# Performance work log

Hardware: AMD Instinct MI355X
Metric: run time of the kernel (lower is better)

## Reference

```python
import jax, jax.numpy as jnp
import numpy as np

# Static config matching init_kwargs
NUM_EXPERTS = 8
CAP_FACTOR = 1.0
MIN_CAP = 8


def setup_inputs() -> dict:
    key = jax.random.key(0)
    ks = jax.random.split(key, 10)
    G, S, D, H, E = 4, 4096, 1024, 4096, NUM_EXPERTS
    s = 0.02  # init stddev like nn.initializers.normal(0.02)
    return {
        "x": jax.random.normal(ks[0], (G, S, D), dtype=jnp.float32),
        "gate": jax.random.normal(ks[1], (D, E), dtype=jnp.float32) * s,
        "W1": jax.random.normal(ks[2], (E, D, H), dtype=jnp.float32) * s,
        "b1": jnp.zeros((E, H), dtype=jnp.float32),
        "W2": jax.random.normal(ks[3], (E, H, D), dtype=jnp.float32) * s,
        "b2": jnp.zeros((E, D), dtype=jnp.float32),
        "Ws1": jax.random.normal(ks[4], (D, H), dtype=jnp.float32) * s,
        "bs1": jnp.zeros((H,), dtype=jnp.float32),
        "Ws2": jax.random.normal(ks[5], (H, D), dtype=jnp.float32) * s,
        "bs2": jnp.zeros((D,), dtype=jnp.float32),
    }


def reference(x, gate, W1, b1, W2, b2, Ws1, bs1, Ws2, bs2):
    G, S, D = x.shape
    E = gate.shape[1]
    T = G * S
    capacity = max(MIN_CAP, int(CAP_FACTOR * T / E))  # static -> 2048

    # ---- Router (inference path: indices + scores, loss = 0) ----
    logits = jnp.einsum('gsd,de->gse', x, gate)           # (G,S,E)
    probs = jax.nn.softmax(logits, axis=-1)
    flat_probs = probs.transpose(2, 0, 1).reshape(E, T)    # (E,T)
    # capacity <= T here, so padding width is 0 (kept implicit)
    scores, token_idx = jax.lax.top_k(flat_probs, k=capacity)  # (E,C)
    scores = jnp.where(scores > -1e8, scores, 0.0)

    # ---- Routed experts: gather -> per-expert FFN (grouped GEMM) -> scatter-add
    flat_x = x.reshape(T, D)
    tok = flat_x[token_idx]                                # (E,C,D) gather
    h = jax.nn.gelu(jnp.einsum('ecd,edh->ech', tok, W1) + b1[:, None, :])
    out_tok = jnp.einsum('ech,ehd->ecd', h, W2) + b2[:, None, :]
    scaled = out_tok * scores[..., None]                   # weight by routing prob
    routed = jnp.zeros_like(flat_x).at[token_idx.reshape(-1)].add(
        scaled.reshape(E * capacity, D)).reshape(G, S, D)

    # ---- Shared expert (single FFN applied to all tokens) ----
    shared = jax.nn.gelu(jnp.einsum('gsd,dh->gsh', x, Ws1) + bs1)
    shared = jnp.einsum('gsh,hd->gsd', shared, Ws2) + bs2

    return routed + shared
```

## Files before the change

kernel.cpp:

```cpp
#include <hip/hip_runtime.h>
#include <hip/hip_bf16.h>

using bf16 = __hip_bfloat16;
typedef short v8s __attribute__((ext_vector_type(8)));
typedef float v4f __attribute__((ext_vector_type(4)));

#define NE 8
#define NT 16384
#define ND 1024
#define NH 4096
#define CAP 2048

__device__ __forceinline__ void load_lds16(const void* g, void* s) {
  __builtin_amdgcn_global_load_lds(
      (const __attribute__((address_space(1))) unsigned int*)g,
      (__attribute__((address_space(3))) unsigned int*)s, 16, 0, 0);
}

__device__ __forceinline__ float gelu_tanh(float x) {
  float u = 0.7978845608028654f * (x + 0.044715f * x * x * x);
  float e = __expf(2.0f * u);
  float t = 1.0f - 2.0f / (e + 1.0f);
  return 0.5f * x * (1.0f + t);
}

__global__ __launch_bounds__(256) void cvt_bf16(const float* __restrict__ s,
                                                bf16* __restrict__ d, int n) {
  for (int i = (blockIdx.x * 256 + threadIdx.x) * 4; i < n; i += gridDim.x * 1024) {
    float4 v = *(const float4*)(s + i);
    bf16 o[4];
    o[0] = __float2bfloat16(v.x); o[1] = __float2bfloat16(v.y);
    o[2] = __float2bfloat16(v.z); o[3] = __float2bfloat16(v.w);
    *(ushort4*)(d + i) = *(ushort4*)o;
  }
}

__global__ __launch_bounds__(256) void tcvt(const float* __restrict__ src,
                                            bf16* __restrict__ dst, int R, int C) {
  __shared__ float tile[32][33];
  size_t mo = (size_t)blockIdx.z * R * C;
  int c0 = blockIdx.x * 32, r0 = blockIdx.y * 32;
  int tx = threadIdx.x & 31, ty = threadIdx.x >> 5;
  for (int i = ty; i < 32; i += 8)
    tile[i][tx] = src[mo + (size_t)(r0 + i) * C + c0 + tx];
  __syncthreads();
  for (int i = ty; i < 32; i += 8)
    dst[mo + (size_t)(c0 + i) * R + r0 + tx] = __float2bfloat16(tile[tx][i]);
}

__global__ __launch_bounds__(256) void router_k(const float* __restrict__ x,
                                                const float* __restrict__ gate,
                                                float* __restrict__ probs) {
  int wave = threadIdx.x >> 6, lane = threadIdx.x & 63;
  int t = blockIdx.x * 4 + wave;
  const float* xr = x + (size_t)t * ND;
  double acc[NE];
#pragma unroll
  for (int e = 0; e < NE; e++) acc[e] = 0.0;
  for (int d = lane; d < ND; d += 64) {
    double xv = (double)xr[d];
    const float* g = gate + d * NE;
#pragma unroll
    for (int e = 0; e < NE; e++) acc[e] += xv * (double)g[e];
  }
#pragma unroll
  for (int e = 0; e < NE; e++) {
    double v = acc[e];
#pragma unroll
    for (int off = 32; off > 0; off >>= 1) v += __shfl_xor(v, off);
    acc[e] = v;
  }
  if (lane == 0) {
    float l[NE], m = -1e30f;
#pragma unroll
    for (int e = 0; e < NE; e++) { l[e] = (float)acc[e]; m = fmaxf(m, l[e]); }
    float p[NE], s = 0.f;
#pragma unroll
    for (int e = 0; e < NE; e++) { p[e] = expf(l[e] - m); s += p[e]; }
#pragma unroll
    for (int e = 0; e < NE; e++) probs[e * NT + t] = p[e] / s;
  }
}

__global__ __launch_bounds__(1024) void topk_k(const float* __restrict__ probs,
                                               unsigned* __restrict__ thr_key,
                                               int* __restrict__ needed) {
  int e = blockIdx.x;
  const float* p = probs + e * NT;
  __shared__ int hist[256];
  __shared__ unsigned s_pref;
  __shared__ int s_rank;
  unsigned prefix = 0;
  int rank = CAP;
  for (int rd = 0; rd < 4; rd++) {
    int shift = 24 - rd * 8;
    if (threadIdx.x < 256) hist[threadIdx.x] = 0;
    __syncthreads();
    unsigned mask = (rd == 0) ? 0u : (0xFFFFFFFFu << (shift + 8));
    for (int t = threadIdx.x; t < NT; t += 1024) {
      unsigned k = __float_as_uint(p[t]);
      if ((k & mask) == prefix) atomicAdd(&hist[(k >> shift) & 255], 1);
    }
    __syncthreads();
    if (threadIdx.x == 0) {
      int cum = 0, b = 255;
      for (;;) {
        int c = hist[b];
        if (cum + c >= rank || b == 0) break;
        cum += c; b--;
      }
      s_pref = prefix | ((unsigned)b << shift);
      s_rank = rank - cum;
    }
    __syncthreads();
    prefix = s_pref; rank = s_rank;
    __syncthreads();
  }
  if (threadIdx.x == 0) { thr_key[e] = prefix; needed[e] = rank; }
}

__global__ void zero_counters(int* p) {
  if (threadIdx.x < 2 * NE) p[threadIdx.x] = 0;
}

__global__ __launch_bounds__(256) void compact_k(const float* __restrict__ probs,
                                                 const unsigned* __restrict__ thr_key,
                                                 const int* __restrict__ needed,
                                                 int* __restrict__ cnt, int* __restrict__ eqc,
                                                 int* __restrict__ tok, float* __restrict__ scr) {
  int gid = blockIdx.x * 256 + threadIdx.x;
  int e = gid >> 14, t = gid & (NT - 1);
  float pv = probs[gid];
  unsigned k = __float_as_uint(pv);
  unsigned thr = thr_key[e];
  int nd = needed[e];
  bool gt = k > thr, eq = k == thr;
  unsigned long long mgt = __ballot(gt), meq = __ballot(eq);
  int lane = threadIdx.x & 63, wv = threadIdx.x >> 6;
  __shared__ int wcnt[2][4];
  __shared__ int base[2];
  if (lane == 0) { wcnt[0][wv] = __popcll(mgt); wcnt[1][wv] = __popcll(meq); }
  __syncthreads();
  if (threadIdx.x == 0) {
    int s0 = wcnt[0][0] + wcnt[0][1] + wcnt[0][2] + wcnt[0][3];
    int s1 = wcnt[1][0] + wcnt[1][1] + wcnt[1][2] + wcnt[1][3];
    base[0] = s0 ? atomicAdd(&cnt[e], s0) : 0;
    base[1] = s1 ? atomicAdd(&eqc[e], s1) : 0;
  }
  __syncthreads();
  unsigned long long lm = (1ull << lane) - 1ull;
  if (gt) {
    int p = __popcll(mgt & lm);
    for (int w = 0; w < wv; w++) p += wcnt[0][w];
    int slot = base[0] + p;
    tok[e * CAP + slot] = t; scr[e * CAP + slot] = pv;
  } else if (eq) {
    int q = base[1] + __popcll(meq & lm);
    for (int w = 0; w < wv; w++) q += wcnt[1][w];
    if (q < nd) {
      int slot = (CAP - nd) + q;
      tok[e * CAP + slot] = t; scr[e * CAP + slot] = pv;
    }
  }
}

#define BAR() __builtin_amdgcn_s_barrier()
#define LGKM0() do { asm volatile("s_waitcnt lgkmcnt(0)" ::: "memory"); \
                     __builtin_amdgcn_sched_barrier(0); } while (0)

template <int MODE>
__global__ __launch_bounds__(512, 2) void gemm256(
    const bf16* __restrict__ A, int lda, const int* __restrict__ rowmap,
    const bf16* __restrict__ BT, long long bstride, int gshift,
    const float* __restrict__ bias, int bias_stride,
    int N, int K,
    bf16* __restrict__ outH, float* __restrict__ outF,
    const int* __restrict__ tok, const float* __restrict__ scr) {
  __shared__ __attribute__((aligned(16))) char lds[131072];
  const int tid = threadIdx.x;
  const int lane = tid & 63, wv = tid >> 6;
  const int wr = wv >> 2, wc = wv & 3;
  const int hw = blockIdx.y * gridDim.x + blockIdx.x;
  const int nwg = gridDim.x * gridDim.y;
  const int swz = (hw & 7) * (nwg >> 3) + (hw >> 3);
  const int m0 = (swz & 63) << 8;
  const int n0 = (swz >> 6) << 8;
  const int grp = m0 >> gshift;
  const bf16* Bp = BT + (size_t)grp * (size_t)bstride;
  const float* bp = bias + (size_t)grp * (size_t)bias_stride;
  const int nt = K >> 6;

  const int srow = tid >> 3;
  const int pc = tid & 7;
  const int gc = pc ^ (srow & 7);
  const bf16* srcA[4]; const bf16* srcB[4];
#pragma unroll
  for (int g = 0; g < 4; g++) {
    int am = m0 + g * 64 + srow;
    int ar = rowmap ? rowmap[am] : am;
    srcA[g] = A + (size_t)ar * lda + gc * 8;
    srcB[g] = Bp + (size_t)(n0 + g * 64 + srow) * K + gc * 8;
  }
  auto stageA = [&](int t, int h) {
    char* d = lds + ((t & 1) * 65536 + h * 16384) + tid * 16;
    load_lds16(srcA[h * 2 + 0] + (size_t)t * 64, d);
    load_lds16(srcA[h * 2 + 1] + (size_t)t * 64, d + 8192);
  };
  auto stageB = [&](int t, int h) {
    char* d = lds + ((t & 1) * 65536 + 32768 + h * 16384) + tid * 16;
    load_lds16(srcB[h * 2 + 0] + (size_t)t * 64, d);
    load_lds16(srcB[h * 2 + 1] + (size_t)t * 64, d + 8192);
  };

  const int fr = lane & 15, hi = lane >> 4;
  const int xr = fr & 7;
  const int cb0 = ((0 + hi) ^ xr) << 4;
  const int cb1 = ((4 + hi) ^ xr) << 4;
  const int arow = ((wr << 7) + fr) << 7;
  const int brow = ((wc << 6) + fr) << 7;

  v4f acc[8][4] = {};
  v8s a[4][2], b[4][2];

#define READ_A(BASE, MOFF)                                                    \
  _Pragma("unroll") for (int mi = 0; mi < 4; mi++) {                          \
    a[mi][0] = *(const v8s*)((BASE) + arow + ((MOFF) + mi) * 2048 + cb0);     \
    a[mi][1] = *(const v8s*)((BASE) + arow + ((MOFF) + mi) * 2048 + cb1);     \
  }
#define READ_B(BASE, NI)                                                      \
  { b[NI][0] = *(const v8s*)((BASE) + brow + (NI) * 2048 + cb0);              \
    b[NI][1] = *(const v8s*)((BASE) + brow + (NI) * 2048 + cb1); }
#define MFMA_QUAD(MOFF, NOFF)                                                 \
  __builtin_amdgcn_s_setprio(1);                                              \
  _Pragma("unroll") for (int kk = 0; kk < 2; kk++)                            \
  _Pragma("unroll") for (int mi = 0; mi < 4; mi++)                            \
  _Pragma("unroll") for (int ni = 0; ni < 2; ni++)                            \
    acc[(MOFF) + mi][(NOFF) + ni] = __builtin_amdgcn_mfma_f32_16x16x32_bf16(  \
        a[mi][kk], b[(NOFF) + ni][kk], acc[(MOFF) + mi][(NOFF) + ni], 0, 0, 0); \
  __builtin_amdgcn_s_setprio(0);

  stageA(0, 0); stageA(0, 1); stageB(0, 0); stageB(0, 1);
  stageA(1, 0); stageA(1, 1); stageB(1, 0); stageB(1, 1);
  asm volatile("s_waitcnt vmcnt(8)" ::: "memory");
  BAR();
  {
    const char* Ab0 = lds; const char* Bb0 = lds + 32768;
    READ_A(Ab0, 0); READ_B(Bb0, 0); READ_B(Bb0, 1);
  }

  for (int t = 0; t < nt; ++t) {
    const char* Ab = lds + (t & 1) * 65536;
    const char* Bb = Ab + 32768;
    const char* AbN = lds + ((t + 1) & 1) * 65536;
    const char* BbN = AbN + 32768;
    LGKM0();
    MFMA_QUAD(0, 0);
    READ_B(Bb, 2); READ_B(Bb, 3);
    stageA(t + 1, 0);
    LGKM0();
    MFMA_QUAD(0, 2);
    READ_A(Ab, 4);
    stageA(t + 1, 1);
    BAR();
    LGKM0();
    MFMA_QUAD(4, 0);
    stageB(t + 2, 0);
    stageB(t + 2, 1);
    asm volatile("s_waitcnt vmcnt(4)" ::: "memory");
    BAR();
    MFMA_QUAD(4, 2);
    READ_A(AbN, 0); READ_B(BbN, 0); READ_B(BbN, 1);
  }
  asm volatile("s_waitcnt vmcnt(0) lgkmcnt(0)" ::: "memory");

  float bv[4];
#pragma unroll
  for (int ni = 0; ni < 4; ni++) bv[ni] = bp[n0 + (wc << 6) + ni * 16 + fr];
  const int rbase = m0 + (wr << 7) + (hi << 2);
#pragma unroll
  for (int mi = 0; mi < 8; mi++) {
#pragma unroll
    for (int r = 0; r < 4; r++) {
      int gm = rbase + mi * 16 + r;
      int trow = 0; float sv = 0.f;
      if (MODE == 2) { trow = tok[gm]; sv = scr[gm]; }
#pragma unroll
      for (int ni = 0; ni < 4; ni++) {
        int gn = n0 + (wc << 6) + ni * 16 + fr;
        float v = acc[mi][ni][r] + bv[ni];
        if (MODE == 0)      outH[(size_t)gm * N + gn] = __float2bfloat16(gelu_tanh(v));
        else if (MODE == 1) outF[(size_t)gm * N + gn] = v;
        else                atomicAdd(outF + (size_t)trow * N + gn, v * sv);
      }
    }
  }
}

extern "C" void kernel_launch(void* const* d_in, const int* in_sizes, int n_in,
                              void* d_out, int out_size, void* d_ws, size_t ws_size,
                              hipStream_t stream) {
  const float* x   = (const float*)d_in[0];
  const float* gate= (const float*)d_in[1];
  const float* W1  = (const float*)d_in[2];
  const float* b1  = (const float*)d_in[3];
  const float* W2  = (const float*)d_in[4];
  const float* b2  = (const float*)d_in[5];
  const float* Ws1 = (const float*)d_in[6];
  const float* bs1 = (const float*)d_in[7];
  const float* Ws2 = (const float*)d_in[8];
  const float* bs2 = (const float*)d_in[9];
  float* out = (float*)d_out;

  char* w = (char*)d_ws;
  size_t off = 0;
  auto alloc = [&](size_t bytes) {
    void* p = w + off;
    off = (off + bytes + 255) & ~(size_t)255;
    return p;
  };
  bf16* xb    = (bf16*)alloc((size_t)NT * ND * 2);
  bf16* w1T   = (bf16*)alloc((size_t)NE * NH * ND * 2);
  bf16* w2T   = (bf16*)alloc((size_t)NE * ND * NH * 2);
  bf16* ws1T  = (bf16*)alloc((size_t)NH * ND * 2);
  bf16* ws2T  = (bf16*)alloc((size_t)ND * NH * 2);
  bf16* h     = (bf16*)alloc((size_t)NT * NH * 2);
  float* probs= (float*)alloc((size_t)NE * NT * 4);
  unsigned* thr = (unsigned*)alloc(NE * 4);
  int* needed = (int*)alloc(NE * 4);
  int* cnt    = (int*)alloc(2 * NE * 4);
  int* eqc    = cnt + NE;
  int* tok    = (int*)alloc((size_t)NE * CAP * 4);
  float* scr  = (float*)alloc((size_t)NE * CAP * 4);
  if (off > ws_size) return;

  cvt_bf16<<<2048, 256, 0, stream>>>(x, xb, NT * ND);
  tcvt<<<dim3(NH / 32, ND / 32, NE), 256, 0, stream>>>(W1, w1T, ND, NH);
  tcvt<<<dim3(ND / 32, NH / 32, NE), 256, 0, stream>>>(W2, w2T, NH, ND);
  tcvt<<<dim3(NH / 32, ND / 32, 1), 256, 0, stream>>>(Ws1, ws1T, ND, NH);
  tcvt<<<dim3(ND / 32, NH / 32, 1), 256, 0, stream>>>(Ws2, ws2T, NH, ND);

  router_k<<<NT / 4, 256, 0, stream>>>(x, gate, probs);
  topk_k<<<NE, 1024, 0, stream>>>(probs, thr, needed);
  zero_counters<<<1, 64, 0, stream>>>(cnt);
  compact_k<<<NE * NT / 256, 256, 0, stream>>>(probs, thr, needed, cnt, eqc, tok, scr);

  gemm256<0><<<dim3(NH / 256, NT / 256), 512, 0, stream>>>(
      xb, ND, nullptr, ws1T, 0, 30, bs1, 0, NH, ND, h, nullptr, nullptr, nullptr);
  gemm256<1><<<dim3(ND / 256, NT / 256), 512, 0, stream>>>(
      h, NH, nullptr, ws2T, 0, 30, bs2, 0, ND, NH, nullptr, out, nullptr, nullptr);

  gemm256<0><<<dim3(NH / 256, NT / 256), 512, 0, stream>>>(
      xb, ND, tok, w1T, (long long)NH * ND, 11, b1, NH, NH, ND, h, nullptr, nullptr, nullptr);
  gemm256<2><<<dim3(ND / 256, NT / 256), 512, 0, stream>>>(
      h, NH, nullptr, w2T, (long long)ND * NH, 11, b2, ND, ND, NH, nullptr, out, tok, scr);
}
```

Measured before the change: 856.0 us.

## Split GEMM fragment registers and prefetch full next tile under last MFMA quad

The GEMM main loop now keeps separate register sets for A rows 0-3/4-7 and B columns 0-1/2-3. All four fragment groups for the next k-tile are read from LDS while the last MFMA quad runs. Partial lgkmcnt waits replace the full drains before each quad. This lets LDS reads overlap MFMA work instead of stalling between quads. It also guards the staging of later tiles at the loop tail and changes the prologue to stage only B for tile 1, at the cost of more live vector registers under the 2-waves-per-SIMD launch bound.

```diff
diff --git a/kernel.cpp b/kernel.cpp
--- a/kernel.cpp
+++ b/kernel.cpp
@@ -165,8 +165,7 @@
 }
 
 #define BAR() __builtin_amdgcn_s_barrier()
-#define LGKM0() do { asm volatile("s_waitcnt lgkmcnt(0)" ::: "memory"); \
-                     __builtin_amdgcn_sched_barrier(0); } while (0)
+#define SBAR0() __builtin_amdgcn_sched_barrier(0)
 
 template <int MODE>
 __global__ __launch_bounds__(512, 2) void gemm256(
@@ -220,56 +219,67 @@
   const int brow = ((wc << 6) + fr) << 7;
 
   v4f acc[8][4] = {};
-  v8s a[4][2], b[4][2];
-
-#define READ_A(BASE, MOFF)                                                    \
+  v8s a03[4][2], a47[4][2], b01[2][2], b23[2][2];
+
+#define R_A03(BASE)                                                           \
   _Pragma("unroll") for (int mi = 0; mi < 4; mi++) {                          \
-    a[mi][0] = *(const v8s*)((BASE) + arow + ((MOFF) + mi) * 2048 + cb0);     \
-    a[mi][1] = *(const v8s*)((BASE) + arow + ((MOFF) + mi) * 2048 + cb1);     \
-  }
-#define READ_B(BASE, NI)                                                      \
-  { b[NI][0] = *(const v8s*)((BASE) + brow + (NI) * 2048 + cb0);              \
-    b[NI][1] = *(const v8s*)((BASE) + brow + (NI) * 2048 + cb1); }
-#define MFMA_QUAD(MOFF, NOFF)                                                 \
+    a03[mi][0] = *(const v8s*)((BASE) + arow + mi * 2048 + cb0);              \
+    a03[mi][1] = *(const v8s*)((BASE) + arow + mi * 2048 + cb1);              \
+  }
+#define R_A47(BASE)                                                           \
+  _Pragma("unroll") for (int mi = 0; mi < 4; mi++) {                          \
+    a47[mi][0] = *(const v8s*)((BASE) + arow + (4 + mi) * 2048 + cb0);        \
+    a47[mi][1] = *(const v8s*)((BASE) + arow + (4 + mi) * 2048 + cb1);        \
+  }
+#define R_B01(BASE)                                                           \
+  _Pragma("unroll") for (int ni = 0; ni < 2; ni++) {                          \
+    b01[ni][0] = *(const v8s*)((BASE) + brow + ni * 2048 + cb0);              \
+    b01[ni][1] = *(const v8s*)((BASE) + brow + ni * 2048 + cb1);              \
+  }
+#define R_B23(BASE)                                                           \
+  _Pragma("unroll") for (int ni = 0; ni < 2; ni++) {                          \
+    b23[ni][0] = *(const v8s*)((BASE) + brow + (2 + ni) * 2048 + cb0);        \
+    b23[ni][1] = *(const v8s*)((BASE) + brow + (2 + ni) * 2048 + cb1);        \
+  }
+#define MFMA_Q(AB, BB, MOFF, NOFF)                                            \
   __builtin_amdgcn_s_setprio(1);                                              \
   _Pragma("unroll") for (int kk = 0; kk < 2; kk++)                            \
   _Pragma("unroll") for (int mi = 0; mi < 4; mi++)                            \
   _Pragma("unroll") for (int ni = 0; ni < 2; ni++)                            \
     acc[(MOFF) + mi][(NOFF) + ni] = __builtin_amdgcn_mfma_f32_16x16x32_bf16(  \
-        a[mi][kk], b[(NOFF) + ni][kk], acc[(MOFF) + mi][(NOFF) + ni], 0, 0, 0); \
+        AB[mi][kk], BB[ni][kk], acc[(MOFF) + mi][(NOFF) + ni], 0, 0, 0);      \
   __builtin_amdgcn_s_setprio(0);
 
   stageA(0, 0); stageA(0, 1); stageB(0, 0); stageB(0, 1);
-  stageA(1, 0); stageA(1, 1); stageB(1, 0); stageB(1, 1);
-  asm volatile("s_waitcnt vmcnt(8)" ::: "memory");
+  if (nt > 1) { stageB(1, 0); stageB(1, 1); }
+  if (nt > 1) { asm volatile("s_waitcnt vmcnt(4)" ::: "memory"); }
+  else        { asm volatile("s_waitcnt vmcnt(0)" ::: "memory"); }
   BAR();
   {
     const char* Ab0 = lds; const char* Bb0 = lds + 32768;
-    READ_A(Ab0, 0); READ_B(Bb0, 0); READ_B(Bb0, 1);
+    R_A03(Ab0); R_B01(Bb0); R_B23(Bb0); R_A47(Ab0);
   }
 
   for (int t = 0; t < nt; ++t) {
-    const char* Ab = lds + (t & 1) * 65536;
-    const char* Bb = Ab + 32768;
     const char* AbN = lds + ((t + 1) & 1) * 65536;
     const char* BbN = AbN + 32768;
-    LGKM0();
-    MFMA_QUAD(0, 0);
-    READ_B(Bb, 2); READ_B(Bb, 3);
-    stageA(t + 1, 0);
-    LGKM0();
-    MFMA_QUAD(0, 2);
-    READ_A(Ab, 4);
-    stageA(t + 1, 1);
+    asm volatile("s_waitcnt lgkmcnt(12)" ::: "memory"); SBAR0();
+    MFMA_Q(a03, b01, 0, 0);
+    if (t + 1 < nt) stageA(t + 1, 0);
+    asm volatile("s_waitcnt lgkmcnt(8)" ::: "memory"); SBAR0();
+    MFMA_Q(a03, b23, 0, 2);
+    if (t + 1 < nt) stageA(t + 1, 1);
     BAR();
-    LGKM0();
-    MFMA_QUAD(4, 0);
-    stageB(t + 2, 0);
-    stageB(t + 2, 1);
-    asm volatile("s_waitcnt vmcnt(4)" ::: "memory");
+    asm volatile("s_waitcnt lgkmcnt(0)" ::: "memory"); SBAR0();
+    MFMA_Q(a47, b01, 4, 0);
+    if (t + 2 < nt) stageB(t + 2, 0);
+    if (t + 2 < nt) stageB(t + 2, 1);
+    if (t + 2 < nt) { asm volatile("s_waitcnt vmcnt(4)" ::: "memory"); }
+    else            { asm volatile("s_waitcnt vmcnt(0)" ::: "memory"); }
     BAR();
-    MFMA_QUAD(4, 2);
-    READ_A(AbN, 0); READ_B(BbN, 0); READ_B(BbN, 1);
+    if (t + 1 < nt) { R_A03(AbN); R_B01(BbN); }
+    MFMA_Q(a47, b23, 4, 2);
+    if (t + 1 < nt) { R_B23(BbN); R_A47(AbN); }
   }
   asm volatile("s_waitcnt vmcnt(0) lgkmcnt(0)" ::: "memory");
 
```

Result: no change. 845.4 us (-1.2%).
